# Kernel tuning notes

Measured on AMD Instinct MI355X. Metric: run time of the kernel, lower is better.

## Reference

```python
import jax, jax.numpy as jnp
import numpy as np

B, N, D, H = 4, 4096, 1024, 16
HD = D // H


def setup_inputs() -> dict:
    key = jax.random.key(0)
    k_x, k_qkv, k_proj, k_b = jax.random.split(key, 4)
    x = jax.random.normal(k_x, (B, N, D), dtype=jnp.float32)
    # torch nn.Linear weights: (out_features, in_features)
    w_qkv = jax.random.normal(k_qkv, (3 * D, D), dtype=jnp.float32) * (D ** -0.5)
    w_proj = jax.random.normal(k_proj, (D, D), dtype=jnp.float32) * (D ** -0.5)
    b_proj = jax.random.normal(k_b, (D,), dtype=jnp.float32) * 0.01
    return {"x": x, "w_qkv": w_qkv, "w_proj": w_proj, "b_proj": b_proj}


def reference(x, w_qkv, w_proj, b_proj):
    b, n, d = x.shape
    # qkv projection (no bias, qkv_bias=False)
    qkv = x @ w_qkv.T                       # (b, n, 3d)
    qkv = qkv.reshape(b, n, 3, H, HD)
    q, k, v = qkv[:, :, 0], qkv[:, :, 1], qkv[:, :, 2]   # each (b, n, H, HD)
    # Faithful to source: q @ k.transpose(-2,-1) with q,k of shape (b,n,H,HD)
    # -> per-token (H,H) attention across heads, softmax over last (head) axis.
    scale = HD ** -0.5
    attn = jnp.einsum('bnhd,bngd->bnhg', q, k) * scale   # (b, n, H, H)
    attn = jax.nn.softmax(attn, axis=-1)
    o = jnp.einsum('bnhg,bngd->bnhd', attn, v)           # (b, n, H, HD)
    # source: transpose(1,2).reshape(b,n,d) (contiguous copy then reshape)
    o = jnp.swapaxes(o, 1, 2).reshape(b, n, d)
    return o @ w_proj.T + b_proj
```

## Files before the change

kernel.cpp:

```cpp
#include <hip/hip_runtime.h>
#include <hip/hip_bf16.h>
#include <cstdint>
#include <cstddef>

#define NB      4
#define NSEQ    4096
#define DM      1024
#define NTOK    16384
#define QKV_N   3072

typedef __attribute__((ext_vector_type(8))) short short8_t;
typedef __attribute__((ext_vector_type(4))) float f32x4;

static __device__ __forceinline__ unsigned short f2bf(float f) {
    unsigned u = __builtin_bit_cast(unsigned, f);
    u += 0x7fffu + ((u >> 16) & 1u);
    return (unsigned short)(u >> 16);
}

static __device__ __forceinline__ void async16(const void* g, void* l) {
    __builtin_amdgcn_global_load_lds(
        (const __attribute__((address_space(1))) void*)g,
        (__attribute__((address_space(3))) void*)l, 16, 0, 0);
}

__global__ void cvt_all(const float* __restrict__ x,
                        const float* __restrict__ wqkv,
                        const float* __restrict__ wproj,
                        unsigned short* __restrict__ xb,
                        unsigned short* __restrict__ wqkvb,
                        unsigned short* __restrict__ wprojb)
{
    int i = blockIdx.x * blockDim.x + threadIdx.x;
    const float* src; unsigned short* dst; int off;
    if (i < 4194304)      { src = x;     dst = xb;     off = i; }
    else if (i < 4980736) { src = wqkv;  dst = wqkvb;  off = i - 4194304; }
    else                  { src = wproj; dst = wprojb; off = i - 4980736; }
    float4 f = ((const float4*)src)[off];
    unsigned lo = (unsigned)f2bf(f.x) | ((unsigned)f2bf(f.y) << 16);
    unsigned hi = (unsigned)f2bf(f.z) | ((unsigned)f2bf(f.w) << 16);
    ((uint2*)dst)[off] = make_uint2(lo, hi);
}

template <bool BF16_OUT, bool BIAS>
__global__ __launch_bounds__(256)
void gemm_bt(const unsigned short* __restrict__ A,
             const unsigned short* __restrict__ Bm,
             void* __restrict__ Cv,
             const float* __restrict__ bias,
             int M, int N, int K)
{
    __shared__ alignas(16) unsigned short As[2][128 * 32];
    __shared__ alignas(16) unsigned short Bs[2][128 * 32];
    const int t    = threadIdx.x;
    const int lane = t & 63;
    const int quad = lane >> 4;
    const int r16  = lane & 15;
    const int wave = t >> 6;
    const int wm   = (wave >> 1) * 64;
    const int wn   = (wave & 1) * 64;
    const int m0   = blockIdx.y * 128;
    const int n0   = blockIdx.x * 128;

    const int c0 = t, c1 = t + 256;
    const int ra0 = c0 >> 2, ra1 = c1 >> 2;
    const int f0 = (ra0 & 3) ^ ((ra0 >> 2) & 3);
    const int f1 = (ra1 & 3) ^ ((ra1 >> 2) & 3);
    const unsigned short* gA0 = A  + (size_t)(m0 + ra0) * K + (((c0 & 3) ^ f0)) * 8;
    const unsigned short* gA1 = A  + (size_t)(m0 + ra1) * K + (((c1 & 3) ^ f1)) * 8;
    const unsigned short* gB0 = Bm + (size_t)(n0 + ra0) * K + (((c0 & 3) ^ f0)) * 8;
    const unsigned short* gB1 = Bm + (size_t)(n0 + ra1) * K + (((c1 & 3) ^ f1)) * 8;

    const int qa = ((quad ^ ((r16 & 3) ^ ((r16 >> 2) & 3))) * 8);

    f32x4 acc[4][4] = {};

    for (int k0 = 0; k0 < K; k0 += 64) {
        #pragma unroll
        for (int s = 0; s < 2; ++s) {
            const int ks = k0 + s * 32;
            async16(gA0 + ks, &As[s][c0 * 8]);
            async16(gA1 + ks, &As[s][c1 * 8]);
            async16(gB0 + ks, &Bs[s][c0 * 8]);
            async16(gB1 + ks, &Bs[s][c1 * 8]);
        }
        __syncthreads();

        #pragma unroll
        for (int s = 0; s < 2; ++s) {
            short8_t a[4], b[4];
            #pragma unroll
            for (int i = 0; i < 4; ++i)
                a[i] = *(const short8_t*)(&As[s][(wm + i * 16 + r16) * 32 + qa]);
            #pragma unroll
            for (int j = 0; j < 4; ++j)
                b[j] = *(const short8_t*)(&Bs[s][(wn + j * 16 + r16) * 32 + qa]);
            #pragma unroll
            for (int i = 0; i < 4; ++i)
                #pragma unroll
                for (int j = 0; j < 4; ++j)
                    acc[i][j] = __builtin_amdgcn_mfma_f32_16x16x32_bf16(
                        a[i], b[j], acc[i][j], 0, 0, 0);
        }
        __syncthreads();
    }

    #pragma unroll
    for (int i = 0; i < 4; ++i) {
        #pragma unroll
        for (int j = 0; j < 4; ++j) {
            const int col = n0 + wn + j * 16 + r16;
            float bv = 0.f;
            if constexpr (BIAS) bv = bias[col];
            #pragma unroll
            for (int r = 0; r < 4; ++r) {
                const int row = m0 + wm + i * 16 + quad * 4 + r;
                float v = acc[i][j][r] + bv;
                if constexpr (BF16_OUT)
                    ((unsigned short*)Cv)[(size_t)row * N + col] = f2bf(v);
                else
                    ((float*)Cv)[(size_t)row * N + col] = v;
            }
        }
    }
}

__global__ __launch_bounds__(256)
void attn_kernel(const unsigned short* __restrict__ qkv,
                 unsigned short* __restrict__ operm)
{
    __shared__ alignas(16) unsigned short s_qkv[4][QKV_N];
    __shared__ alignas(16) unsigned short s_p[4][256];
    __shared__ alignas(16) unsigned short s_o[4][16 * 72];
    const int t     = threadIdx.x;
    const int lane  = t & 63;
    const int wave  = t >> 6;
    const int quad  = lane >> 4;
    const int r16   = lane & 15;
    const int token = blockIdx.x * 4 + wave;

    {
        const unsigned short* src = qkv + (size_t)token * QKV_N;
        #pragma unroll
        for (int i = 0; i < 6; ++i)
            async16(src + i * 512 + lane * 8, &s_qkv[wave][i * 512 + lane * 8]);
    }
    __syncthreads();

    const unsigned short* q  = &s_qkv[wave][0];
    const unsigned short* kk = q + 1024;
    const unsigned short* vv = q + 2048;

    f32x4 s = {};
    #pragma unroll
    for (int c = 0; c < 64; c += 32) {
        short8_t aq = *(const short8_t*)(q  + r16 * 64 + c + quad * 8);
        short8_t bk = *(const short8_t*)(kk + r16 * 64 + c + quad * 8);
        s = __builtin_amdgcn_mfma_f32_16x16x32_bf16(aq, bk, s, 0, 0, 0);
    }

    #pragma unroll
    for (int r = 0; r < 4; ++r) {
        float x = s[r] * 0.125f;
        float m = x;
        #pragma unroll
        for (int o = 1; o < 16; o <<= 1) m = fmaxf(m, __shfl_xor(m, o));
        float e = __expf(x - m);
        float su = e;
        #pragma unroll
        for (int o = 1; o < 16; o <<= 1) su += __shfl_xor(su, o);
        s_p[wave][(quad * 4 + r) * 16 + r16] = f2bf(e * __builtin_amdgcn_rcpf(su));
    }
    __syncthreads();

    short8_t pa = {};
    if (quad < 2) pa = *(const short8_t*)(&s_p[wave][r16 * 16 + quad * 8]);

    f32x4 o[4];
    #pragma unroll
    for (int j = 0; j < 4; ++j) {
        short8_t vb = {};
        if (quad < 2) {
            #pragma unroll
            for (int e = 0; e < 8; ++e)
                vb[e] = (short)vv[(quad * 8 + e) * 64 + j * 16 + r16];
        }
        f32x4 z = {};
        o[j] = __builtin_amdgcn_mfma_f32_16x16x32_bf16(pa, vb, z, 0, 0, 0);
    }

    #pragma unroll
    for (int j = 0; j < 4; ++j)
        #pragma unroll
        for (int r = 0; r < 4; ++r)
            s_o[wave][(quad * 4 + r) * 72 + j * 16 + r16] = f2bf(o[j][r]);
    __syncthreads();

    const int b    = token >> 12;
    const int npos = token & 4095;
    const size_t base = (size_t)b * (NSEQ * DM)
                      + (size_t)(npos >> 4) * 1024
                      + (size_t)(npos & 15) * 64;
    #pragma unroll
    for (int c = lane; c < 128; c += 64) {
        const int h = c >> 3, part = c & 7;
        int4 val = *(const int4*)(&s_o[wave][h * 72 + part * 8]);
        *(int4*)(operm + base + (size_t)h * (256 * 1024) + part * 8) = val;
    }
}

extern "C" void kernel_launch(void* const* d_in, const int* in_sizes, int n_in,
                              void* d_out, int out_size, void* d_ws, size_t ws_size,
                              hipStream_t stream)
{
    const float* x      = (const float*)d_in[0];
    const float* w_qkv  = (const float*)d_in[1];
    const float* w_proj = (const float*)d_in[2];
    const float* b_proj = (const float*)d_in[3];
    float* out = (float*)d_out;

    unsigned short* xb     = (unsigned short*)d_ws;
    unsigned short* wqkvb  = xb     + (size_t)16777216;
    unsigned short* wprojb = wqkvb  + (size_t)3145728;
    unsigned short* qkvb   = wprojb + (size_t)1048576;
    unsigned short* opermb = qkvb   + (size_t)50331648;

    cvt_all<<<20480, 256, 0, stream>>>(x, w_qkv, w_proj, xb, wqkvb, wprojb);

    dim3 g1(QKV_N / 128, NTOK / 128);
    gemm_bt<true, false><<<g1, 256, 0, stream>>>(xb, wqkvb, qkvb, nullptr,
                                                 NTOK, QKV_N, DM);

    attn_kernel<<<NTOK / 4, 256, 0, stream>>>(qkvb, opermb);

    dim3 g2(DM / 128, NTOK / 128);
    gemm_bt<false, true><<<g2, 256, 0, stream>>>(opermb, wprojb, out, b_proj,
                                                 NTOK, DM, DM);
}
```

Measured before the change: 331.6 us.

## Replace 128x128 GEMM with 256x256 tile, 8-wave pipelined double-buffered kernel

Both GEMMs move from a 128x128, 4-wave tile to a 256x256, 8-wave tile with a K-step of 64. Global-to-LDS async loads for tile g+2 are interleaved with the MFMA phases of tile g, with explicit vmcnt waits, barriers and setprio. The kernel also uses an XOR LDS swizzle and a grouped block-index remap for L2 locality. The larger tile roughly doubles arithmetic intensity per LDS load and hides load latency. The cost is heavy register pressure (128 accumulator floats per lane) and fewer blocks, only 256 for the projection GEMM, which may underfill the CUs.

```diff
diff --git a/kernel.cpp b/kernel.cpp
--- a/kernel.cpp
+++ b/kernel.cpp
@@ -43,83 +43,136 @@
 }
 
 template <bool BF16_OUT, bool BIAS>
-__global__ __launch_bounds__(256)
-void gemm_bt(const unsigned short* __restrict__ A,
+__global__ __launch_bounds__(512, 2)
+void gemm256(const unsigned short* __restrict__ A,
              const unsigned short* __restrict__ Bm,
              void* __restrict__ Cv,
              const float* __restrict__ bias,
              int M, int N, int K)
 {
-    __shared__ alignas(16) unsigned short As[2][128 * 32];
-    __shared__ alignas(16) unsigned short Bs[2][128 * 32];
+    __shared__ alignas(16) unsigned short As[2][16384];
+    __shared__ alignas(16) unsigned short Bs[2][16384];
+
     const int t    = threadIdx.x;
     const int lane = t & 63;
+    const int wave = t >> 6;
     const int quad = lane >> 4;
     const int r16  = lane & 15;
-    const int wave = t >> 6;
-    const int wm   = (wave >> 1) * 64;
-    const int wn   = (wave & 1) * 64;
-    const int m0   = blockIdx.y * 128;
-    const int n0   = blockIdx.x * 128;
-
-    const int c0 = t, c1 = t + 256;
-    const int ra0 = c0 >> 2, ra1 = c1 >> 2;
-    const int f0 = (ra0 & 3) ^ ((ra0 >> 2) & 3);
-    const int f1 = (ra1 & 3) ^ ((ra1 >> 2) & 3);
-    const unsigned short* gA0 = A  + (size_t)(m0 + ra0) * K + (((c0 & 3) ^ f0)) * 8;
-    const unsigned short* gA1 = A  + (size_t)(m0 + ra1) * K + (((c1 & 3) ^ f1)) * 8;
-    const unsigned short* gB0 = Bm + (size_t)(n0 + ra0) * K + (((c0 & 3) ^ f0)) * 8;
-    const unsigned short* gB1 = Bm + (size_t)(n0 + ra1) * K + (((c1 & 3) ^ f1)) * 8;
-
-    const int qa = ((quad ^ ((r16 & 3) ^ ((r16 >> 2) & 3))) * 8);
-
-    f32x4 acc[4][4] = {};
-
-    for (int k0 = 0; k0 < K; k0 += 64) {
-        #pragma unroll
-        for (int s = 0; s < 2; ++s) {
-            const int ks = k0 + s * 32;
-            async16(gA0 + ks, &As[s][c0 * 8]);
-            async16(gA1 + ks, &As[s][c1 * 8]);
-            async16(gB0 + ks, &Bs[s][c0 * 8]);
-            async16(gB1 + ks, &Bs[s][c1 * 8]);
-        }
-        __syncthreads();
-
-        #pragma unroll
-        for (int s = 0; s < 2; ++s) {
-            short8_t a[4], b[4];
-            #pragma unroll
-            for (int i = 0; i < 4; ++i)
-                a[i] = *(const short8_t*)(&As[s][(wm + i * 16 + r16) * 32 + qa]);
-            #pragma unroll
-            for (int j = 0; j < 4; ++j)
-                b[j] = *(const short8_t*)(&Bs[s][(wn + j * 16 + r16) * 32 + qa]);
-            #pragma unroll
-            for (int i = 0; i < 4; ++i)
-                #pragma unroll
-                for (int j = 0; j < 4; ++j)
-                    acc[i][j] = __builtin_amdgcn_mfma_f32_16x16x32_bf16(
-                        a[i], b[j], acc[i][j], 0, 0, 0);
-        }
-        __syncthreads();
-    }
-
-    #pragma unroll
-    for (int i = 0; i < 4; ++i) {
-        #pragma unroll
-        for (int j = 0; j < 4; ++j) {
-            const int col = n0 + wn + j * 16 + r16;
+    const int wm   = wave >> 2;
+    const int wn   = wave & 3;
+
+    const int nwg = gridDim.x;
+    const int swz = (blockIdx.x & 7) * (nwg >> 3) + (blockIdx.x >> 3);
+    const int ntn = N >> 8;
+    const int tm  = swz / ntn, tn = swz - tm * ntn;
+    const int m0  = tm << 8, n0 = tn << 8;
+
+    const int srow = t >> 3;
+    const int schk = ((t & 7) ^ (srow & 7)) << 3;
+    const unsigned short* gA = A  + (size_t)(m0 + srow) * K + schk;
+    const unsigned short* gB = Bm + (size_t)(n0 + srow) * K + schk;
+    unsigned short* const lA = &As[0][0] + t * 8;
+    unsigned short* const lB = &Bs[0][0] + t * 8;
+
+    const int NT = K >> 6;
+
+#define STA(buf, kt, r) async16(gA + (size_t)(r) * 64 * K + (size_t)(kt) * 64, \
+                                lA + (buf) * 16384 + (r) * 4096)
+#define STB(buf, kt, r) async16(gB + (size_t)(r) * 64 * K + (size_t)(kt) * 64, \
+                                lB + (buf) * 16384 + (r) * 4096)
+
+    const int cs0 = ((quad    ) ^ (r16 & 7)) << 3;
+    const int cs1 = ((quad ^ 4) ^ (r16 & 7)) << 3;
+    const int aRow = wm * 128 + r16;
+    const int bRow = wn * 64  + r16;
+
+    f32x4 acc[8][4] = {};
+
+    STA(0,0,0); STA(0,0,1); STA(0,0,2); STA(0,0,3);
+    STB(0,0,0); STB(0,0,1); STB(0,0,2); STB(0,0,3);
+    STA(1,1,0); STA(1,1,1); STA(1,1,2); STA(1,1,3);
+    STB(1,1,0); STB(1,1,1); STB(1,1,2); STB(1,1,3);
+    asm volatile("s_waitcnt vmcnt(8)" ::: "memory");
+    __builtin_amdgcn_s_barrier();
+
+#define RD_A(QR) _Pragma("unroll") for (int ii = 0; ii < 4; ++ii) {            \
+        a[ii][0] = *(const short8_t*)(Ab + (aRow + (QR)*64 + ii*16) * 64 + cs0); \
+        a[ii][1] = *(const short8_t*)(Ab + (aRow + (QR)*64 + ii*16) * 64 + cs1); }
+#define RD_B(bb, QC) _Pragma("unroll") for (int jj = 0; jj < 2; ++jj) {        \
+        bb[jj][0] = *(const short8_t*)(Bb + (bRow + (QC)*32 + jj*16) * 64 + cs0); \
+        bb[jj][1] = *(const short8_t*)(Bb + (bRow + (QC)*32 + jj*16) * 64 + cs1); }
+#define MM(QR, QC, bb) _Pragma("unroll") for (int s = 0; s < 2; ++s)           \
+      _Pragma("unroll") for (int ii = 0; ii < 4; ++ii)                          \
+        _Pragma("unroll") for (int jj = 0; jj < 2; ++jj)                        \
+          acc[(QR)*4+ii][(QC)*2+jj] = __builtin_amdgcn_mfma_f32_16x16x32_bf16( \
+              a[ii][s], bb[jj][s], acc[(QR)*4+ii][(QC)*2+jj], 0, 0, 0);
+#define SYNC_PRE  __builtin_amdgcn_s_barrier();                                \
+                  asm volatile("s_waitcnt lgkmcnt(0)" ::: "memory");           \
+                  __builtin_amdgcn_sched_barrier(0);                           \
+                  __builtin_amdgcn_s_setprio(1);
+#define SYNC_POST __builtin_amdgcn_s_setprio(0);                               \
+                  __builtin_amdgcn_s_barrier();                                \
+                  asm volatile("" ::: "memory");
+
+    for (int g = 0; g < NT; ++g) {
+        const int cur = g & 1;
+        const unsigned short* Ab = &As[cur][0];
+        const unsigned short* Bb = &Bs[cur][0];
+        const bool pf = (g + 2 < NT);
+        short8_t a[4][2], b0[2][2], b1[2][2];
+
+        RD_A(0) RD_B(b0, 0)
+        SYNC_PRE
+        MM(0, 0, b0)
+        SYNC_POST
+
+        RD_B(b1, 1)
+        if (pf) { STA(cur, g+2, 0); STA(cur, g+2, 2); }
+        SYNC_PRE
+        MM(0, 1, b1)
+        SYNC_POST
+
+        RD_A(1)
+        if (pf) { STB(cur, g+2, 0); STB(cur, g+2, 1); }
+        SYNC_PRE
+        MM(1, 0, b0)
+        SYNC_POST
+
+        if (pf) { STA(cur, g+2, 1); STA(cur, g+2, 3);
+                  STB(cur, g+2, 2); STB(cur, g+2, 3); }
+        __builtin_amdgcn_s_barrier();
+        __builtin_amdgcn_s_setprio(1);
+        MM(1, 1, b1)
+        __builtin_amdgcn_s_setprio(0);
+        if (pf)              asm volatile("s_waitcnt vmcnt(8)" ::: "memory");
+        else if (g + 1 < NT) asm volatile("s_waitcnt vmcnt(0)" ::: "memory");
+        __builtin_amdgcn_s_barrier();
+        asm volatile("" ::: "memory");
+    }
+
+#undef STA
+#undef STB
+#undef RD_A
+#undef RD_B
+#undef MM
+#undef SYNC_PRE
+#undef SYNC_POST
+
+    #pragma unroll
+    for (int ri = 0; ri < 8; ++ri) {
+        const int row = m0 + wm * 128 + (ri >> 2) * 64 + (ri & 3) * 16 + quad * 4;
+        #pragma unroll
+        for (int cj = 0; cj < 4; ++cj) {
+            const int col = n0 + wn * 64 + (cj >> 1) * 32 + (cj & 1) * 16 + r16;
             float bv = 0.f;
             if constexpr (BIAS) bv = bias[col];
             #pragma unroll
             for (int r = 0; r < 4; ++r) {
-                const int row = m0 + wm + i * 16 + quad * 4 + r;
-                float v = acc[i][j][r] + bv;
+                float v = acc[ri][cj][r] + bv;
                 if constexpr (BF16_OUT)
-                    ((unsigned short*)Cv)[(size_t)row * N + col] = f2bf(v);
+                    ((unsigned short*)Cv)[(size_t)(row + r) * N + col] = f2bf(v);
                 else
-                    ((float*)Cv)[(size_t)row * N + col] = v;
+                    ((float*)Cv)[(size_t)(row + r) * N + col] = v;
             }
         }
     }
@@ -227,13 +280,11 @@
 
     cvt_all<<<20480, 256, 0, stream>>>(x, w_qkv, w_proj, xb, wqkvb, wprojb);
 
-    dim3 g1(QKV_N / 128, NTOK / 128);
-    gemm_bt<true, false><<<g1, 256, 0, stream>>>(xb, wqkvb, qkvb, nullptr,
-                                                 NTOK, QKV_N, DM);
+    gemm256<true, false><<<768, 512, 0, stream>>>(xb, wqkvb, qkvb, nullptr,
+                                                  NTOK, QKV_N, DM);
 
     attn_kernel<<<NTOK / 4, 256, 0, stream>>>(qkvb, opermb);
 
-    dim3 g2(DM / 128, NTOK / 128);
-    gemm_bt<false, true><<<g2, 256, 0, stream>>>(opermb, wprojb, out, b_proj,
-                                                 NTOK, DM, DM);
-}
+    gemm256<false, true><<<256, 512, 0, stream>>>(opermb, wprojb, out, b_proj,
+                                                  NTOK, DM, DM);
+}
```

Result: faster. 302.1 us (-8.9%).
